# Kernel optimization log

Measured on AMD Instinct MI355X. Metric: run time of the kernel, lower is better.

Reference implementation:

```python
import jax, jax.numpy as jnp
import numpy as np

NUM_HEADS = 12
TOPK = 90


def setup_inputs() -> dict:
    key = jax.random.key(0)
    k1, k2, k3 = jax.random.split(key, 3)
    B, N, C = 8, 512, 768
    x = jax.random.normal(k1, (B, N, C), dtype=jnp.float32)
    qkv_w = jax.random.normal(k2, (3 * C, C), dtype=jnp.float32) * (C ** -0.5)
    proj_w = jax.random.normal(k3, (C, C), dtype=jnp.float32) * (C ** -0.5)
    proj_b = jnp.zeros((C,), dtype=jnp.float32)
    return {"x": x, "qkv_w": qkv_w, "proj_w": proj_w, "proj_b": proj_b, "islast": 0}


def reference(x, qkv_w, proj_w, proj_b, islast):
    B, N, C = x.shape
    H = NUM_HEADS
    hd = C // H
    scale = hd ** -0.5
    # qkv projection (no bias), split into q,k,v heads: [B,H,N,hd]
    qkv = (x @ qkv_w.T).reshape(B, N, 3, H, hd).transpose(2, 0, 3, 1, 4)
    q, k, v = qkv[0], qkv[1], qkv[2]
    attn = jnp.einsum('bhnd,bhmd->bhnm', q, k) * scale  # [B,H,N,N]
    if not islast:
        # keep only the top-k scores per row (kth-value threshold == topk mask)
        kth = jax.lax.top_k(attn, TOPK)[0][..., -1:]  # [B,H,N,1]
        attn = jnp.where(attn >= kth, attn, -jnp.inf)
    attn = jax.nn.softmax(attn, axis=-1)
    out = jnp.einsum('bhnm,bhmd->bnhd', attn, v).reshape(B, N, C)
    out = out @ proj_w.T + proj_b
    return out, attn
```

## Files before the change

kernel.cpp:

```cpp
#include <hip/hip_runtime.h>
#include <math.h>

#define BB 8
#define NN 512
#define CC 768
#define HH 12
#define HD 64
#define TOPK 90
#define QKV_ELEMS (BB*HH*NN*HD)
#define KC 2304

typedef __attribute__((ext_vector_type(8))) short short8;
typedef __attribute__((ext_vector_type(4))) float floatx4;

__device__ inline unsigned short f2bf(float f) {
    unsigned int u = __float_as_uint(f);
    u += 0x7FFFu + ((u >> 16) & 1u);
    return (unsigned short)(u >> 16);
}
__device__ inline float bf2f(unsigned short h) {
    return __uint_as_float(((unsigned int)h) << 16);
}

template<bool IS_A>
__global__ __launch_bounds__(256) void split_k(const float* __restrict__ in,
                                               unsigned short* __restrict__ o2,
                                               int total) {
    int idx = blockIdx.x * 256 + threadIdx.x;
    if (idx >= total) return;
    int e = idx * 4;
    int m = e / CC, kk = e - m * CC;
    float4 f = *(const float4*)(in + e);
    ushort4 hi, lo;
    hi.x = f2bf(f.x); lo.x = f2bf(f.x - bf2f(hi.x));
    hi.y = f2bf(f.y); lo.y = f2bf(f.y - bf2f(hi.y));
    hi.z = f2bf(f.z); lo.z = f2bf(f.z - bf2f(hi.z));
    hi.w = f2bf(f.w); lo.w = f2bf(f.w - bf2f(hi.w));
    unsigned short* base = o2 + (size_t)m * KC + kk;
    *(ushort4*)(base)        = hi;
    *(ushort4*)(base + CC)   = IS_A ? hi : lo;
    *(ushort4*)(base + 2*CC) = IS_A ? lo : hi;
}

template<int NCOLS, bool QKV_EPI>
__global__ __launch_bounds__(256) void gemm_split(const unsigned short* __restrict__ A,
                                                  const unsigned short* __restrict__ Bm,
                                                  const float* __restrict__ bias,
                                                  float* __restrict__ out,
                                                  unsigned short* __restrict__ qh,
                                                  unsigned short* __restrict__ ql,
                                                  unsigned short* __restrict__ kh,
                                                  unsigned short* __restrict__ kl,
                                                  float* __restrict__ vt) {
    __shared__ char lds[16384];
    const int bm = blockIdx.x, bn = blockIdx.y;
    const int tid  = threadIdx.x;
    const int wave = tid >> 6, lane = tid & 63;
    const int wm = wave >> 1, wn = wave & 1;
    const int quad = lane >> 4, r = lane & 15;

    const int cA0 = tid, cA1 = tid + 256;
    const int mA0 = cA0 >> 2, oA0 = (cA0 & 3) ^ ((mA0 >> 1) & 3);
    const int mA1 = cA1 >> 2, oA1 = (cA1 & 3) ^ ((mA1 >> 1) & 3);
    const unsigned short* gA0 = A  + (size_t)(bm*128 + mA0) * KC + oA0*8;
    const unsigned short* gA1 = A  + (size_t)(bm*128 + mA1) * KC + oA1*8;
    const unsigned short* gB0 = Bm + (size_t)(bn*128 + mA0) * KC + oA0*8;
    const unsigned short* gB1 = Bm + (size_t)(bn*128 + mA1) * KC + oA1*8;
    char* lA0 = lds + (wave*64)*16;
    char* lA1 = lds + (256 + wave*64)*16;
    char* lB0 = lds + 8192 + (wave*64)*16;
    char* lB1 = lds + 8192 + (256 + wave*64)*16;

    const int octsel = quad ^ ((r >> 1) & 3);
    int aoff[4], boff[4];
#pragma unroll
    for (int i = 0; i < 4; ++i) {
        aoff[i] = ((wm*64 + i*16 + r)*4 + octsel) * 16;
        boff[i] = 8192 + ((wn*64 + i*16 + r)*4 + octsel) * 16;
    }

    floatx4 acc[4][4];
#pragma unroll
    for (int i = 0; i < 4; ++i)
#pragma unroll
        for (int j = 0; j < 4; ++j)
            acc[i][j] = (floatx4){0.f, 0.f, 0.f, 0.f};

    for (int it = 0; it < KC/32; ++it) {
        __syncthreads();
        __builtin_amdgcn_global_load_lds((const __attribute__((address_space(1))) unsigned int*)gA0,
                                         (__attribute__((address_space(3))) unsigned int*)lA0, 16, 0, 0);
        __builtin_amdgcn_global_load_lds((const __attribute__((address_space(1))) unsigned int*)gA1,
                                         (__attribute__((address_space(3))) unsigned int*)lA1, 16, 0, 0);
        __builtin_amdgcn_global_load_lds((const __attribute__((address_space(1))) unsigned int*)gB0,
                                         (__attribute__((address_space(3))) unsigned int*)lB0, 16, 0, 0);
        __builtin_amdgcn_global_load_lds((const __attribute__((address_space(1))) unsigned int*)gB1,
                                         (__attribute__((address_space(3))) unsigned int*)lB1, 16, 0, 0);
        gA0 += 32; gA1 += 32; gB0 += 32; gB1 += 32;
        asm volatile("s_waitcnt vmcnt(0)" ::: "memory");
        __syncthreads();

        short8 af[4], bf[4];
#pragma unroll
        for (int i = 0; i < 4; ++i) af[i] = *(const short8*)(lds + aoff[i]);
#pragma unroll
        for (int j = 0; j < 4; ++j) bf[j] = *(const short8*)(lds + boff[j]);
#pragma unroll
        for (int i = 0; i < 4; ++i)
#pragma unroll
            for (int j = 0; j < 4; ++j)
                acc[i][j] = __builtin_amdgcn_mfma_f32_16x16x32_bf16(af[i], bf[j], acc[i][j], 0, 0, 0);
    }

    if (QKV_EPI) {
#pragma unroll
        for (int j = 0; j < 4; ++j) {
            int col = bn*128 + wn*64 + j*16 + r;
            int t = col / CC;
            int rem = col - t*CC;
            int h = rem >> 6, d = rem & 63;
            if (t == 2) {
#pragma unroll
                for (int i = 0; i < 4; ++i) {
                    int m0 = bm*128 + wm*64 + i*16 + quad*4;
                    int b = m0 >> 9, n0 = m0 & 511;
                    float4 o4 = {acc[i][j][0], acc[i][j][1], acc[i][j][2], acc[i][j][3]};
                    *(float4*)(vt + ((size_t)((b*HH + h)*HD + d))*NN + n0) = o4;
                }
            } else {
                unsigned short* ph = (t == 0) ? qh : kh;
                unsigned short* pl = (t == 0) ? ql : kl;
#pragma unroll
                for (int i = 0; i < 4; ++i) {
#pragma unroll
                    for (int e = 0; e < 4; ++e) {
                        int m = bm*128 + wm*64 + i*16 + quad*4 + e;
                        int b = m >> 9, nrow = m & 511;
                        size_t idx = ((size_t)(b*HH + h)*NN + nrow)*HD + d;
                        float val = acc[i][j][e];
                        unsigned short hi = f2bf(val);
                        ph[idx] = hi;
                        pl[idx] = f2bf(val - bf2f(hi));
                    }
                }
            }
        }
    } else {
#pragma unroll
        for (int j = 0; j < 4; ++j) {
            int col = bn*128 + wn*64 + j*16 + r;
            float bv = bias[col];
#pragma unroll
            for (int i = 0; i < 4; ++i) {
#pragma unroll
                for (int e = 0; e < 4; ++e) {
                    int m = bm*128 + wm*64 + i*16 + quad*4 + e;
                    out[(size_t)m*NCOLS + col] = acc[i][j][e] + bv;
                }
            }
        }
    }
}

__global__ __launch_bounds__(256) void attn_scores_k(
        const unsigned short* __restrict__ qh, const unsigned short* __restrict__ ql,
        const unsigned short* __restrict__ kh, const unsigned short* __restrict__ kl,
        const int* __restrict__ islast, float* __restrict__ attn) {

    __shared__ unsigned short qs[2][64][72];
    __shared__ char ks[16384];

    const int bh = blockIdx.x >> 3;
    const int rb = blockIdx.x & 7;
    const int tid = threadIdx.x;
    const int wv = tid >> 6, lane = tid & 63;
    const int quad = lane >> 4, r = lane & 15;

    const unsigned short* gq[2] = { qh + ((size_t)bh*NN + rb*64)*HD,
                                    ql + ((size_t)bh*NN + rb*64)*HD };
#pragma unroll
    for (int i = 0; i < 4; ++i) {
        int s = tid + i*256;
        int hl = s >> 9, s2 = s & 511;
        int row = s2 >> 3, oct = s2 & 7;
        short8 val = *(const short8*)(gq[hl] + row*HD + oct*8);
        *(short8*)&qs[hl][row][oct*8] = val;
    }
    __syncthreads();

    short8 afr[6];
    {
        const int arow = wv*16 + r;
#pragma unroll
        for (int t = 0; t < 3; ++t) {
            int src = (t == 2) ? 1 : 0;
#pragma unroll
            for (int half = 0; half < 2; ++half)
                afr[t*2+half] = *(const short8*)&qs[src][arow][half*32 + quad*8];
        }
    }

    floatx4 acc[32];
#pragma unroll
    for (int ct = 0; ct < 32; ++ct) acc[ct] = (floatx4){0.f,0.f,0.f,0.f};

    const unsigned short* gk[2] = { kh + (size_t)bh*NN*HD, kl + (size_t)bh*NN*HD };

    for (int ch = 0; ch < 8; ++ch) {
        __syncthreads();
#pragma unroll
        for (int i = 0; i < 4; ++i) {
            int s = tid + i*256;
            int hl = s >> 9, s2 = s & 511;
            int row = s2 >> 3, octp = s2 & 7;
            int oct = octp ^ (row & 7);
            const unsigned short* src = gk[hl] + (size_t)(ch*64 + row)*HD + oct*8;
            __builtin_amdgcn_global_load_lds(
                (const __attribute__((address_space(1))) unsigned int*)src,
                (__attribute__((address_space(3))) unsigned int*)(ks + (size_t)(i*256 + wv*64)*16),
                16, 0, 0);
        }
        asm volatile("s_waitcnt vmcnt(0)" ::: "memory");
        __syncthreads();

#pragma unroll
        for (int ctl = 0; ctl < 4; ++ctl) {
            const int ct = ch*4 + ctl;
            const int n = ctl*16 + r;
#pragma unroll
            for (int t = 0; t < 3; ++t) {
                const int srcB = (t == 1) ? 1 : 0;
#pragma unroll
                for (int half = 0; half < 2; ++half) {
                    const int oct = (half*4 + quad) ^ (n & 7);
                    short8 bfr = *(const short8*)(ks + srcB*8192 + n*128 + oct*16);
                    acc[ct] = __builtin_amdgcn_mfma_f32_16x16x32_bf16(afr[t*2+half], bfr, acc[ct], 0, 0, 0);
                }
            }
        }
    }

#pragma unroll
    for (int ct = 0; ct < 32; ++ct) acc[ct] *= 0.125f;

    const int last = islast[0];

#pragma unroll
    for (int e = 0; e < 4; ++e) {
#pragma unroll
        for (int ct = 0; ct < 32; ++ct) {
            unsigned int t = __float_as_uint(acc[ct][e]);
            t = (t & 0x80000000u) ? ~t : (t | 0x80000000u);
            acc[ct][e] = __uint_as_float(t);
        }
        unsigned int key = 0u;
        if (!last) {
            unsigned int am = 0xFFFFFFFFu;
            int kk = TOPK, cntA = 512, done = 0;
            for (int bit = 31; bit >= 0; --bit) {
                if (!done) {
                    unsigned int m1 = 0u;
#pragma unroll
                    for (int ct = 0; ct < 32; ++ct)
                        m1 |= ((__float_as_uint(acc[ct][e]) >> bit) & 1u) << ct;
                    int c1 = __popc(am & m1);
                    c1 += __shfl_xor(c1, 1);
                    c1 += __shfl_xor(c1, 2);
                    c1 += __shfl_xor(c1, 4);
                    c1 += __shfl_xor(c1, 8);
                    if (kk <= c1) { am &= m1; cntA = c1; }
                    else          { kk -= c1; am &= ~m1; cntA -= c1; }
                    done = (cntA == kk) | (kk == 1);
                }
                if (__ballot(!done) == 0ull) break;
            }
            unsigned int mn = 0xFFFFFFFFu, mx = 0u;
#pragma unroll
            for (int ct = 0; ct < 32; ++ct) {
                unsigned int uu = __float_as_uint(acc[ct][e]);
                if ((am >> ct) & 1u) { mn = mn < uu ? mn : uu; mx = mx > uu ? mx : uu; }
            }
#pragma unroll
            for (int off = 1; off <= 8; off <<= 1) {
                unsigned int mns = __shfl_xor(mn, off), mxs = __shfl_xor(mx, off);
                mn = mn < mns ? mn : mns; mx = mx > mxs ? mx : mxs;
            }
            key = (kk == 1) ? mx : mn;
        }

        unsigned int umx = 0u;
#pragma unroll
        for (int ct = 0; ct < 32; ++ct) {
            unsigned int uu = __float_as_uint(acc[ct][e]);
            umx = umx > uu ? umx : uu;
        }
#pragma unroll
        for (int off = 1; off <= 8; off <<= 1) {
            unsigned int t2 = __shfl_xor(umx, off);
            umx = umx > t2 ? umx : t2;
        }
        float fmx = __uint_as_float((umx & 0x80000000u) ? (umx & 0x7FFFFFFFu) : ~umx);
        float sum = 0.f;
#pragma unroll
        for (int ct = 0; ct < 32; ++ct) {
            unsigned int uu = __float_as_uint(acc[ct][e]);
            float f = __uint_as_float((uu & 0x80000000u) ? (uu & 0x7FFFFFFFu) : ~uu);
            float ev = (last || uu >= key) ? __expf(f - fmx) : 0.f;
            acc[ct][e] = ev;
            sum += ev;
        }
#pragma unroll
        for (int off = 1; off <= 8; off <<= 1) sum += __shfl_xor(sum, off);
        const float inv = 1.f / sum;
        float* arow = attn + ((size_t)bh*NN + rb*64 + wv*16 + quad*4 + e) * NN;
#pragma unroll
        for (int ct = 0; ct < 32; ++ct) arow[ct*16 + r] = acc[ct][e] * inv;
    }
}

__global__ __launch_bounds__(256) void attn_pv_k(const float* __restrict__ attn,
                                                 const float* __restrict__ vt,
                                                 unsigned short* __restrict__ Ao) {
    __shared__ unsigned short pls[64][72];
    __shared__ unsigned short vhs[64][72];
    __shared__ unsigned short vls[64][72];

    const int blk = blockIdx.x;
    const int bh  = blk >> 3;
    const int rb  = blk & 7;
    const int b = bh / HH, h = bh % HH;
    const int tid = threadIdx.x;
    const int wv = tid >> 6, lane = tid & 63;
    const int quad = lane >> 4, r = lane & 15;

    const int sm = tid >> 2;
    const int sk = (tid & 3) * 16;
    const float* prow = attn + ((size_t)bh*NN + rb*64 + sm) * NN + sk;
    const float* vrow = vt + ((size_t)bh*HD + sm) * NN + sk;

    floatx4 accO[4];
#pragma unroll
    for (int j = 0; j < 4; ++j) accO[j] = (floatx4){0.f,0.f,0.f,0.f};

    for (int ch = 0; ch < 8; ++ch) {
        float pv[16], vv[16];
#pragma unroll
        for (int x = 0; x < 4; ++x) {
            *(float4*)&pv[x*4] = *(const float4*)(prow + ch*64 + x*4);
            *(float4*)&vv[x*4] = *(const float4*)(vrow + ch*64 + x*4);
        }
        __syncthreads();
        unsigned short tp[16], th[16], tl[16];
#pragma unroll
        for (int x = 0; x < 16; ++x) {
            tp[x] = f2bf(pv[x]);
            th[x] = f2bf(vv[x]);
            tl[x] = f2bf(vv[x] - bf2f(th[x]));
        }
        *(short8*)&pls[sm][sk]   = *(short8*)&tp[0];
        *(short8*)&pls[sm][sk+8] = *(short8*)&tp[8];
        *(short8*)&vhs[sm][sk]   = *(short8*)&th[0];
        *(short8*)&vhs[sm][sk+8] = *(short8*)&th[8];
        *(short8*)&vls[sm][sk]   = *(short8*)&tl[0];
        *(short8*)&vls[sm][sk+8] = *(short8*)&tl[8];
        __syncthreads();

#pragma unroll
        for (int kb = 0; kb < 2; ++kb) {
            short8 af = *(const short8*)&pls[wv*16 + r][kb*32 + quad*8];
#pragma unroll
            for (int j = 0; j < 4; ++j) {
                short8 bh8 = *(const short8*)&vhs[j*16 + r][kb*32 + quad*8];
                short8 bl8 = *(const short8*)&vls[j*16 + r][kb*32 + quad*8];
                accO[j] = __builtin_amdgcn_mfma_f32_16x16x32_bf16(af, bh8, accO[j], 0, 0, 0);
                accO[j] = __builtin_amdgcn_mfma_f32_16x16x32_bf16(af, bl8, accO[j], 0, 0, 0);
            }
        }
    }

#pragma unroll
    for (int j = 0; j < 4; ++j) {
        int d = j*16 + r;
#pragma unroll
        for (int e = 0; e < 4; ++e) {
            int n = rb*64 + wv*16 + quad*4 + e;
            size_t mrow = (size_t)b*NN + n;
            float val = accO[j][e];
            unsigned short hi = f2bf(val);
            unsigned short lo = f2bf(val - bf2f(hi));
            unsigned short* base = Ao + mrow*KC + h*HD + d;
            base[0] = hi; base[CC] = hi; base[2*CC] = lo;
        }
    }
}

extern "C" void kernel_launch(void* const* d_in, const int* in_sizes, int n_in,
                              void* d_out, int out_size, void* d_ws, size_t ws_size,
                              hipStream_t stream) {
    const float* x      = (const float*)d_in[0];
    const float* qkv_w  = (const float*)d_in[1];
    const float* proj_w = (const float*)d_in[2];
    const float* proj_b = (const float*)d_in[3];
    const int*   islast = (const int*)d_in[4];

    float* out  = (float*)d_out;
    float* attn = out + (size_t)BB*NN*CC;

    float* ws = (float*)d_ws;
    float* vt = ws;
    unsigned short* qhp = (unsigned short*)(ws + (size_t)QKV_ELEMS);
    unsigned short* qlp = qhp + (size_t)QKV_ELEMS;
    unsigned short* khp = qlp + (size_t)QKV_ELEMS;
    unsigned short* klp = khp + (size_t)QKV_ELEMS;
    unsigned short* Asp   = klp + (size_t)QKV_ELEMS;
    unsigned short* Bqkv  = Asp  + (size_t)4096*KC;
    unsigned short* Bproj = Bqkv + (size_t)2304*KC;

    split_k<true> <<<dim3(4096*CC/4/256), 256, 0, stream>>>(x,      Asp,   4096*CC/4);
    split_k<false><<<dim3(2304*CC/4/256), 256, 0, stream>>>(qkv_w,  Bqkv,  2304*CC/4);
    split_k<false><<<dim3(CC*CC/4/256),   256, 0, stream>>>(proj_w, Bproj, CC*CC/4);

    gemm_split<0, true>  <<<dim3(32, 18), 256, 0, stream>>>(Asp, Bqkv, nullptr, nullptr,
                                                            qhp, qlp, khp, klp, vt);
    attn_scores_k        <<<dim3(96*8),   256, 0, stream>>>(qhp, qlp, khp, klp, islast, attn);
    attn_pv_k            <<<dim3(96*8),   256, 0, stream>>>(attn, vt, Asp);
    gemm_split<CC, false><<<dim3(32, 6),  256, 0, stream>>>(Asp, Bproj, proj_b, out,
                                                            nullptr, nullptr, nullptr, nullptr, nullptr);
}
```

Measured before the change: 393.7 us.

## Skip common high bits in top-k radix select and remap block order

The radix select for the per-row top-k threshold now starts at the highest bit that differs across the row, found from the OR and AND of all the keys, so bit positions shared by every element are skipped. Ordered keys are kept in a separate array instead of being written back into the accumulators, with the scale folded into the conversion. Block index mapping in the scores and PV kernels is switched so consecutive blocks cover different batch-heads, and scores gets launch_bounds min-blocks 1. The key array may raise register pressure, and the new mapping changes cache locality.

```diff
diff --git a/kernel.cpp b/kernel.cpp
--- a/kernel.cpp
+++ b/kernel.cpp
@@ -162,7 +162,7 @@
     }
 }
 
-__global__ __launch_bounds__(256) void attn_scores_k(
+__global__ __launch_bounds__(256, 1) void attn_scores_k(
         const unsigned short* __restrict__ qh, const unsigned short* __restrict__ ql,
         const unsigned short* __restrict__ kh, const unsigned short* __restrict__ kl,
         const int* __restrict__ islast, float* __restrict__ attn) {
@@ -170,8 +170,8 @@
     __shared__ unsigned short qs[2][64][72];
     __shared__ char ks[16384];
 
-    const int bh = blockIdx.x >> 3;
-    const int rb = blockIdx.x & 7;
+    const int bh = blockIdx.x % 96;
+    const int rb = blockIdx.x / 96;
     const int tid = threadIdx.x;
     const int wv = tid >> 6, lane = tid & 63;
     const int quad = lane >> 4, r = lane & 15;
@@ -240,29 +240,38 @@
         }
     }
 
-#pragma unroll
-    for (int ct = 0; ct < 32; ++ct) acc[ct] *= 0.125f;
-
-    const int last = islast[0];
+    const int lastv = islast[0];
 
 #pragma unroll
     for (int e = 0; e < 4; ++e) {
+        unsigned int key[32];
 #pragma unroll
         for (int ct = 0; ct < 32; ++ct) {
-            unsigned int t = __float_as_uint(acc[ct][e]);
-            t = (t & 0x80000000u) ? ~t : (t | 0x80000000u);
-            acc[ct][e] = __uint_as_float(t);
-        }
-        unsigned int key = 0u;
-        if (!last) {
+            unsigned int t = __float_as_uint(acc[ct][e] * 0.125f);
+            key[ct] = (t & 0x80000000u) ? ~t : (t | 0x80000000u);
+        }
+
+        unsigned int kth = 0u;
+        if (!lastv) {
+            unsigned int uo = key[0], ua = key[0];
+#pragma unroll
+            for (int ct = 1; ct < 32; ++ct) { uo |= key[ct]; ua &= key[ct]; }
+#pragma unroll
+            for (int off = 1; off <= 8; off <<= 1) {
+                uo |= __shfl_xor(uo, off);
+                ua &= __shfl_xor(ua, off);
+            }
+            unsigned int diff = uo ^ ua;
+            int bit = 31 - __clz(diff);
             unsigned int am = 0xFFFFFFFFu;
-            int kk = TOPK, cntA = 512, done = 0;
-            for (int bit = 31; bit >= 0; --bit) {
+            int kk = TOPK, cntA = 512;
+            int done = (diff == 0u);
+            while (__ballot(!done) != 0ull) {
                 if (!done) {
                     unsigned int m1 = 0u;
 #pragma unroll
                     for (int ct = 0; ct < 32; ++ct)
-                        m1 |= ((__float_as_uint(acc[ct][e]) >> bit) & 1u) << ct;
+                        m1 |= ((key[ct] >> bit) & 1u) << ct;
                     int c1 = __popc(am & m1);
                     c1 += __shfl_xor(c1, 1);
                     c1 += __shfl_xor(c1, 2);
@@ -270,30 +279,29 @@
                     c1 += __shfl_xor(c1, 8);
                     if (kk <= c1) { am &= m1; cntA = c1; }
                     else          { kk -= c1; am &= ~m1; cntA -= c1; }
-                    done = (cntA == kk) | (kk == 1);
-                }
-                if (__ballot(!done) == 0ull) break;
+                    --bit;
+                    done = (cntA == kk) | (kk == 1) | (bit < 0);
+                }
             }
             unsigned int mn = 0xFFFFFFFFu, mx = 0u;
 #pragma unroll
             for (int ct = 0; ct < 32; ++ct) {
-                unsigned int uu = __float_as_uint(acc[ct][e]);
-                if ((am >> ct) & 1u) { mn = mn < uu ? mn : uu; mx = mx > uu ? mx : uu; }
+                if ((am >> ct) & 1u) {
+                    mn = mn < key[ct] ? mn : key[ct];
+                    mx = mx > key[ct] ? mx : key[ct];
+                }
             }
 #pragma unroll
             for (int off = 1; off <= 8; off <<= 1) {
                 unsigned int mns = __shfl_xor(mn, off), mxs = __shfl_xor(mx, off);
                 mn = mn < mns ? mn : mns; mx = mx > mxs ? mx : mxs;
             }
-            key = (kk == 1) ? mx : mn;
-        }
-
-        unsigned int umx = 0u;
-#pragma unroll
-        for (int ct = 0; ct < 32; ++ct) {
-            unsigned int uu = __float_as_uint(acc[ct][e]);
-            umx = umx > uu ? umx : uu;
-        }
+            kth = (kk == 1) ? mx : mn;
+        }
+
+        unsigned int umx = key[0];
+#pragma unroll
+        for (int ct = 1; ct < 32; ++ct) umx = umx > key[ct] ? umx : key[ct];
 #pragma unroll
         for (int off = 1; off <= 8; off <<= 1) {
             unsigned int t2 = __shfl_xor(umx, off);
@@ -303,9 +311,9 @@
         float sum = 0.f;
 #pragma unroll
         for (int ct = 0; ct < 32; ++ct) {
-            unsigned int uu = __float_as_uint(acc[ct][e]);
+            unsigned int uu = key[ct];
             float f = __uint_as_float((uu & 0x80000000u) ? (uu & 0x7FFFFFFFu) : ~uu);
-            float ev = (last || uu >= key) ? __expf(f - fmx) : 0.f;
+            float ev = (lastv || uu >= kth) ? __expf(f - fmx) : 0.f;
             acc[ct][e] = ev;
             sum += ev;
         }
@@ -326,8 +334,8 @@
     __shared__ unsigned short vls[64][72];
 
     const int blk = blockIdx.x;
-    const int bh  = blk >> 3;
-    const int rb  = blk & 7;
+    const int bh  = blk % 96;
+    const int rb  = blk / 96;
     const int b = bh / HH, h = bh % HH;
     const int tid = threadIdx.x;
     const int wv = tid >> 6, lane = tid & 63;
```

After: 366.2 us. 7.0% less time.
